# Optimization experiments

Hardware: AMD Instinct MI355X
Metric: run time of the kernel (lower is better)

## Reference

```python
import jax, jax.numpy as jnp
import numpy as np

SEQ = 8192      # sequence_size
EMB = 64        # embedSize
NCLS = 2        # numClasses
NLEAF = 8192    # leaves of a perfect binary tree (13 levels)


def setup_inputs() -> dict:
    key = jax.random.key(0)
    ks = jax.random.split(key, 7)
    s = 0.02  # small init scale so 13 stacked relu-linears stay numerically sane
    return {
        "leaf_seqs": jax.random.normal(ks[0], (NLEAF, SEQ), jnp.float32),
        "emb_W": jax.random.normal(ks[1], (EMB, SEQ), jnp.float32) * s,
        "emb_b": jax.random.normal(ks[2], (EMB,), jnp.float32) * s,
        "W_W": jax.random.normal(ks[3], (EMB, 2 * EMB), jnp.float32) * s,
        "W_b": jax.random.normal(ks[4], (EMB,), jnp.float32) * s,
        "proj_W": jax.random.normal(ks[5], (NCLS, EMB), jnp.float32) * s,
        "proj_b": jax.random.normal(ks[6], (NCLS,), jnp.float32) * s,
    }


def reference(leaf_seqs, emb_W, emb_b, W_W, W_b, proj_W, proj_b):
    # Leaves: relu(embedding(seq)) for every leaf, batched. [NLEAF, EMB]
    h = jax.nn.relu(jnp.einsum('ns,es->ne', leaf_seqs, emb_W) + emb_b)
    # Internal nodes: combine adjacent sibling pairs level by level
    # (left-to-right recursion over a perfect binary tree == adjacent pairing).
    depth = int(np.log2(NLEAF))  # 13 levels, static Python loop
    for _ in range(depth):
        pair = jnp.concatenate([h[0::2], h[1::2]], axis=1)  # [N/2, 2*EMB]
        h = jax.nn.relu(jnp.einsum('nc,ec->ne', pair, W_W) + W_b)
    # Root: projection logits, [1, NCLS] (forward() only emits the root).
    return jnp.einsum('ne,ce->nc', h, proj_W) + proj_b
```

## Files before the change

### kernel.cpp

```cpp
#include <hip/hip_runtime.h>

#define SEQ   8192
#define EMB   64
#define NLEAF 8192
#define KQ    2048
#define KT    64
#define NT    (KQ / KT)

typedef __attribute__((ext_vector_type(4))) float        f32x4;
typedef __attribute__((ext_vector_type(4))) unsigned int u32x4;

__device__ __forceinline__ unsigned rne_pair(float x, float y) {
    const unsigned ux = __float_as_uint(x), uy = __float_as_uint(y);
    const unsigned rx = (ux + 0x7fffu + ((ux >> 16) & 1u)) >> 16;
    const unsigned ry = (uy + 0x7fffu + ((uy >> 16) & 1u)) & 0xffff0000u;
    return rx | ry;
}

__device__ __forceinline__ void mfma16(f32x4& d, const u32x4 a, const u32x4 b) {
    asm("v_mfma_f32_16x16x32_bf16 %0, %1, %2, %0" : "+v"(d) : "v"(a), "v"(b));
}

__device__ __forceinline__ u32x4 frag_rne(const float* buf, int row, int kk) {
    const int c = kk >> 2;
    const int s = row & 7;
    const char* base = (const char*)buf + row * 256;
    const f32x4 v0 = *(const f32x4*)(base + 16 * (c ^ s));
    const f32x4 v1 = *(const f32x4*)(base + 16 * ((c + 1) ^ s));
    u32x4 h;
    h[0] = rne_pair(v0.x, v0.y);
    h[1] = rne_pair(v0.z, v0.w);
    h[2] = rne_pair(v1.x, v1.y);
    h[3] = rne_pair(v1.z, v1.w);
    return h;
}

#define GLDS16(gp, lp) \
    __builtin_amdgcn_global_load_lds( \
        (const __attribute__((address_space(1))) void*)(gp), \
        (__attribute__((address_space(3))) void*)(lp), 16, 0, 0)

__global__ __launch_bounds__(256) void k_cvtW(const float* __restrict__ W,
                                              unsigned* __restrict__ Wt)
{
    const int gid  = blockIdx.x * 256 + threadIdx.x;
    const int chsw = gid & 7;
    const int row  = (gid >> 3) & 63;
    const int t    = (gid >> 9) & 31;
    const int q    = gid >> 14;
    const int c    = chsw ^ (row & 7);
    const float* src = W + (size_t)row * SEQ + q * KQ + t * KT + c * 8;
    const f32x4 a = *(const f32x4*)(src);
    const f32x4 b = *(const f32x4*)(src + 4);
    u32x4 v;
    v[0] = rne_pair(a.x, a.y);
    v[1] = rne_pair(a.z, a.w);
    v[2] = rne_pair(b.x, b.y);
    v[3] = rne_pair(b.z, b.w);
    u32x4* dst = (u32x4*)(Wt + ((q * 32 + t) * 512 + row * 8 + chsw) * 4);
    *dst = v;
}

__global__ __launch_bounds__(256, 2) void k_gemm(
        const float* __restrict__ A, const char* __restrict__ Wt,
        float* __restrict__ P)
{
    __shared__ float sA[3][64 * 64];
    __shared__ char  sW[3][8192];

    const int tid  = threadIdx.x;
    const int lane = tid & 63;
    const int wid  = tid >> 6;

    const int g     = blockIdx.x >> 2;
    const int q     = blockIdx.x & 3;
    const int gl0   = g * 64;
    const int kbase = q * KQ;

    const int lr = lane >> 4;
    const int lc = lane & 15;

    const float* pA0;
    const float* pA1;
    const float* pA2;
    const float* pA3;
    {
        const int r0 = wid * 16 + 0 * 4 + lr;
        const int r1 = wid * 16 + 1 * 4 + lr;
        const int r2 = wid * 16 + 2 * 4 + lr;
        const int r3 = wid * 16 + 3 * 4 + lr;
        pA0 = A + (size_t)(gl0 + r0) * SEQ + kbase + (lc ^ (r0 & 7)) * 4;
        pA1 = A + (size_t)(gl0 + r1) * SEQ + kbase + (lc ^ (r1 & 7)) * 4;
        pA2 = A + (size_t)(gl0 + r2) * SEQ + kbase + (lc ^ (r2 & 7)) * 4;
        pA3 = A + (size_t)(gl0 + r3) * SEQ + kbase + (lc ^ (r3 & 7)) * 4;
    }
    const char* pW = Wt + (size_t)(q * 32) * 8192 + (2 * wid) * 1024 + lane * 16;

    const int fr = lane & 15;
    const int fq = lane >> 4;

    f32x4 acc0 = {0.f, 0.f, 0.f, 0.f};
    f32x4 acc1 = {0.f, 0.f, 0.f, 0.f};
    f32x4 acc2 = {0.f, 0.f, 0.f, 0.f};
    f32x4 acc3 = {0.f, 0.f, 0.f, 0.f};

#define STAGE(bi_) do { \
    char* wdst = (char*)&sW[bi_][0] + 2 * wid * 1024; \
    GLDS16(pW, wdst); \
    GLDS16(pW + 1024, wdst + 1024); \
    pW += 8192; \
    GLDS16(pA0, &sA[bi_][(wid * 16 + 0) * 64]); \
    GLDS16(pA1, &sA[bi_][(wid * 16 + 4) * 64]); \
    GLDS16(pA2, &sA[bi_][(wid * 16 + 8) * 64]); \
    GLDS16(pA3, &sA[bi_][(wid * 16 + 12) * 64]); \
    pA0 += KT; pA1 += KT; pA2 += KT; pA3 += KT; \
} while (0)

#define COMPUTE(bi_) do { \
    const float* bufA_ = &sA[bi_][0]; \
    const char*  bufW_ = &sW[bi_][0]; \
    _Pragma("unroll") \
    for (int k32 = 0; k32 < 2; ++k32) { \
        const u32x4 af = frag_rne(bufA_, wid * 16 + fr, k32 * 32 + fq * 8); \
        const int baddr = fr * 128 + 16 * ((k32 * 4 + fq) ^ (fr & 7)); \
        const u32x4 b0 = *(const u32x4*)(bufW_ + baddr); \
        const u32x4 b1 = *(const u32x4*)(bufW_ + 2048 + baddr); \
        const u32x4 b2 = *(const u32x4*)(bufW_ + 4096 + baddr); \
        const u32x4 b3 = *(const u32x4*)(bufW_ + 6144 + baddr); \
        mfma16(acc0, af, b0); \
        mfma16(acc1, af, b1); \
        mfma16(acc2, af, b2); \
        mfma16(acc3, af, b3); \
    } \
} while (0)

    STAGE(0);
    STAGE(1);

    int bcur = 0, bnxt = 1, bfut = 2;
    #pragma unroll 1
    for (int t = 0; t < NT; ++t) {
        if (t + 1 < NT) asm volatile("s_waitcnt vmcnt(6)" ::: "memory");
        else            asm volatile("s_waitcnt vmcnt(0)" ::: "memory");
        __builtin_amdgcn_s_barrier();
        __builtin_amdgcn_sched_barrier(0);
        if (t + 2 < NT) STAGE(bfut);
        COMPUTE(bcur);
        const int tmp = bcur; bcur = bnxt; bnxt = bfut; bfut = tmp;
    }

#undef STAGE
#undef COMPUTE

    float* Pq = P + (size_t)q * NLEAF * EMB;
    const int row0 = gl0 + wid * 16 + fq * 4;
    #pragma unroll
    for (int r = 0; r < 4; ++r) {
        Pq[(size_t)(row0 + r) * EMB +  0 + fr] = acc0[r];
        Pq[(size_t)(row0 + r) * EMB + 16 + fr] = acc1[r];
        Pq[(size_t)(row0 + r) * EMB + 32 + fr] = acc2[r];
        Pq[(size_t)(row0 + r) * EMB + 48 + fr] = acc3[r];
    }
}

__device__ __forceinline__ void load_Wt(float (*Wt)[132],
                                        const float* __restrict__ WW, int tid) {
    const int e  = tid >> 2;
    const int c0 = (tid & 3) * 32;
    #pragma unroll
    for (int j = 0; j < 32; j += 4)
        *(f32x4*)&Wt[e][c0 + j] = *(const f32x4*)&WW[e * 128 + c0 + j];
}

__device__ __forceinline__ float hsum4(const f32x4 a) {
    return a.x + a.y + a.z + a.w;
}

__device__ __forceinline__ float* tree_levels(float* bufA, float* bufB,
        const float (*Wt)[132], float wb, int n0, int nlv, int tid)
{
    const int lane = tid & 63;
    const int wid  = tid >> 6;
    float* src = bufA;
    float* dst = bufB;
    int n = n0;
    for (int lvl = 0; lvl < nlv; ++lvl) {
        const int nodes = n >> 1;
        for (int base = wid * 4; base < nodes; base += 16) {
            const int cnt = (nodes - base < 4) ? (nodes - base) : 4;
            if (cnt == 4) {
                f32x4 ac0 = {0.f,0.f,0.f,0.f}, ac1 = ac0, ac2 = ac0, ac3 = ac0;
                const float* x0 = src + (2 * (base + 0)) * 68;
                const float* x1 = src + (2 * (base + 1)) * 68;
                const float* x2 = src + (2 * (base + 2)) * 68;
                const float* x3 = src + (2 * (base + 3)) * 68;
                #pragma unroll
                for (int j = 0; j < 32; ++j) {
                    const f32x4 w4 = *(const f32x4*)&Wt[lane][4 * j];
                    const int off = (j < 16) ? (4 * j) : (68 + 4 * (j - 16));
                    ac0 += w4 * *(const f32x4*)(x0 + off);
                    ac1 += w4 * *(const f32x4*)(x1 + off);
                    ac2 += w4 * *(const f32x4*)(x2 + off);
                    ac3 += w4 * *(const f32x4*)(x3 + off);
                }
                dst[(base + 0) * 68 + lane] = fmaxf(wb + hsum4(ac0), 0.f);
                dst[(base + 1) * 68 + lane] = fmaxf(wb + hsum4(ac1), 0.f);
                dst[(base + 2) * 68 + lane] = fmaxf(wb + hsum4(ac2), 0.f);
                dst[(base + 3) * 68 + lane] = fmaxf(wb + hsum4(ac3), 0.f);
            } else {
                for (int u = 0; u < cnt; ++u) {
                    f32x4 ac = {0.f, 0.f, 0.f, 0.f};
                    const float* x = src + (2 * (base + u)) * 68;
                    #pragma unroll
                    for (int j = 0; j < 32; ++j) {
                        const f32x4 w4 = *(const f32x4*)&Wt[lane][4 * j];
                        const int off = (j < 16) ? (4 * j) : (68 + 4 * (j - 16));
                        ac += w4 * *(const f32x4*)(x + off);
                    }
                    dst[(base + u) * 68 + lane] = fmaxf(wb + hsum4(ac), 0.f);
                }
            }
        }
        __syncthreads();
        float* tswp = src; src = dst; dst = tswp;
        n = nodes;
    }
    return src;
}

__global__ __launch_bounds__(256) void k_tree32(const float* __restrict__ P,
        const float* __restrict__ eb, const float* __restrict__ WW,
        const float* __restrict__ Wb, float* __restrict__ roots)
{
    __shared__ float hA[32][68];
    __shared__ float hB[16][68];
    __shared__ float Wt[64][132];
    const int tid = threadIdx.x;
    const int b   = blockIdx.x;
    load_Wt(Wt, WW, tid);
    {
        const int lf = tid >> 3;
        const int e0 = (tid & 7) * 8;
        const size_t base = (size_t)(b * 32 + lf) * EMB + e0;
        f32x4 s0 = *(const f32x4*)&P[base];
        f32x4 s1 = *(const f32x4*)&P[base + 4];
        s0 += *(const f32x4*)&P[(size_t)1 * NLEAF * EMB + base];
        s1 += *(const f32x4*)&P[(size_t)1 * NLEAF * EMB + base + 4];
        s0 += *(const f32x4*)&P[(size_t)2 * NLEAF * EMB + base];
        s1 += *(const f32x4*)&P[(size_t)2 * NLEAF * EMB + base + 4];
        s0 += *(const f32x4*)&P[(size_t)3 * NLEAF * EMB + base];
        s1 += *(const f32x4*)&P[(size_t)3 * NLEAF * EMB + base + 4];
        s0 += *(const f32x4*)&eb[e0];
        s1 += *(const f32x4*)&eb[e0 + 4];
        s0.x = fmaxf(s0.x, 0.f); s0.y = fmaxf(s0.y, 0.f);
        s0.z = fmaxf(s0.z, 0.f); s0.w = fmaxf(s0.w, 0.f);
        s1.x = fmaxf(s1.x, 0.f); s1.y = fmaxf(s1.y, 0.f);
        s1.z = fmaxf(s1.z, 0.f); s1.w = fmaxf(s1.w, 0.f);
        *(f32x4*)&hA[lf][e0]     = s0;
        *(f32x4*)&hA[lf][e0 + 4] = s1;
    }
    const float wb = Wb[tid & 63];
    __syncthreads();
    float* root = tree_levels(&hA[0][0], &hB[0][0], Wt, wb, 32, 5, tid);
    if (tid < 64) roots[b * 64 + tid] = root[tid];
}

__global__ __launch_bounds__(256) void k_tree16(const float* __restrict__ in,
        const float* __restrict__ WW, const float* __restrict__ Wb,
        float* __restrict__ outv)
{
    __shared__ float hA[32][68];
    __shared__ float hB[16][68];
    __shared__ float Wt[64][132];
    const int tid = threadIdx.x;
    load_Wt(Wt, WW, tid);
    {
        const int r  = tid >> 4;
        const int e0 = (tid & 15) * 4;
        *(f32x4*)&hA[r][e0] =
            *(const f32x4*)&in[(size_t)(blockIdx.x * 16 + r) * EMB + e0];
    }
    const float wb = Wb[tid & 63];
    __syncthreads();
    float* root = tree_levels(&hA[0][0], &hB[0][0], Wt, wb, 16, 4, tid);
    if (tid < 64) outv[blockIdx.x * 64 + tid] = root[tid];
}

__global__ __launch_bounds__(256) void k_root(const float* __restrict__ in,
        const float* __restrict__ WW, const float* __restrict__ Wb,
        const float* __restrict__ pW, const float* __restrict__ pb,
        float* __restrict__ out)
{
    __shared__ float hA[32][68];
    __shared__ float hB[16][68];
    __shared__ float Wt[64][132];
    const int tid = threadIdx.x;
    load_Wt(Wt, WW, tid);
    {
        const int r  = tid >> 4;
        const int e0 = (tid & 15) * 4;
        *(f32x4*)&hA[r][e0] = *(const f32x4*)&in[(size_t)r * EMB + e0];
    }
    const float wb = Wb[tid & 63];
    __syncthreads();
    float* root = tree_levels(&hA[0][0], &hB[0][0], Wt, wb, 16, 4, tid);
    if (tid < 64) {
        const float hv = root[tid];
        float t0 = hv * pW[tid];
        float t1 = hv * pW[64 + tid];
        #pragma unroll
        for (int off = 32; off > 0; off >>= 1) {
            t0 += __shfl_down(t0, off);
            t1 += __shfl_down(t1, off);
        }
        if (tid == 0) { out[0] = t0 + pb[0]; out[1] = t1 + pb[1]; }
    }
}

extern "C" void kernel_launch(void* const* d_in, const int* in_sizes, int n_in,
                              void* d_out, int out_size, void* d_ws, size_t ws_size,
                              hipStream_t stream)
{
    const float* A  = (const float*)d_in[0];
    const float* eW = (const float*)d_in[1];
    const float* eb = (const float*)d_in[2];
    const float* WW = (const float*)d_in[3];
    const float* Wb = (const float*)d_in[4];
    const float* pW = (const float*)d_in[5];
    const float* pb = (const float*)d_in[6];
    float* out = (float*)d_out;

    float* P     = (float*)d_ws;
    float* roots = P + (size_t)4 * NLEAF * EMB;
    float* l9    = roots + 256 * EMB;
    char*  Wtil  = (char*)d_ws + (size_t)16 * 1024 * 1024;

    k_cvtW  <<<dim3(256), dim3(256), 0, stream>>>(eW, (unsigned*)Wtil);
    k_gemm  <<<dim3(512), dim3(256), 0, stream>>>(A, Wtil, P);
    k_tree32<<<dim3(256), dim3(256), 0, stream>>>(P, eb, WW, Wb, roots);
    k_tree16<<<dim3(16),  dim3(256), 0, stream>>>(roots, WW, Wb, l9);
    k_root  <<<dim3(1),   dim3(256), 0, stream>>>(l9, WW, Wb, pW, pb, out);
}
```

Before: 82.58 us.

## Fuse last two tree kernels via atomic last-block-done and transpose W smem layout

```diff
diff --git a/kernel.cpp b/kernel.cpp
--- a/kernel.cpp
+++ b/kernel.cpp
@@ -163,13 +163,15 @@
     }
 }
 
-__device__ __forceinline__ void load_Wt(float (*Wt)[132],
-                                        const float* __restrict__ WW, int tid) {
-    const int e  = tid >> 2;
-    const int c0 = (tid & 3) * 32;
+__device__ __forceinline__ void load_WtV(f32x4 (*WtV)[64],
+                                         const float* __restrict__ WW, int tid) {
+    const int e  = tid & 63;
+    const int jg = tid >> 6;
     #pragma unroll
-    for (int j = 0; j < 32; j += 4)
-        *(f32x4*)&Wt[e][c0 + j] = *(const f32x4*)&WW[e * 128 + c0 + j];
+    for (int u = 0; u < 8; ++u) {
+        const int j = jg * 8 + u;
+        WtV[j][e] = *(const f32x4*)&WW[e * 128 + 4 * j];
+    }
 }
 
 __device__ __forceinline__ float hsum4(const f32x4 a) {
@@ -177,7 +179,7 @@
 }
 
 __device__ __forceinline__ float* tree_levels(float* bufA, float* bufB,
-        const float (*Wt)[132], float wb, int n0, int nlv, int tid)
+        const f32x4 (*WtV)[64], float wb, int n0, int nlv, int tid)
 {
     const int lane = tid & 63;
     const int wid  = tid >> 6;
@@ -196,7 +198,7 @@
                 const float* x3 = src + (2 * (base + 3)) * 68;
                 #pragma unroll
                 for (int j = 0; j < 32; ++j) {
-                    const f32x4 w4 = *(const f32x4*)&Wt[lane][4 * j];
+                    const f32x4 w4 = WtV[j][lane];
                     const int off = (j < 16) ? (4 * j) : (68 + 4 * (j - 16));
                     ac0 += w4 * *(const f32x4*)(x0 + off);
                     ac1 += w4 * *(const f32x4*)(x1 + off);
@@ -213,7 +215,7 @@
                     const float* x = src + (2 * (base + u)) * 68;
                     #pragma unroll
                     for (int j = 0; j < 32; ++j) {
-                        const f32x4 w4 = *(const f32x4*)&Wt[lane][4 * j];
+                        const f32x4 w4 = WtV[j][lane];
                         const int off = (j < 16) ? (4 * j) : (68 + 4 * (j - 16));
                         ac += w4 * *(const f32x4*)(x + off);
                     }
@@ -234,10 +236,10 @@
 {
     __shared__ float hA[32][68];
     __shared__ float hB[16][68];
-    __shared__ float Wt[64][132];
+    __shared__ f32x4 WtV[32][64];
     const int tid = threadIdx.x;
     const int b   = blockIdx.x;
-    load_Wt(Wt, WW, tid);
+    load_WtV(WtV, WW, tid);
     {
         const int lf = tid >> 3;
         const int e0 = (tid & 7) * 8;
@@ -261,19 +263,22 @@
     }
     const float wb = Wb[tid & 63];
     __syncthreads();
-    float* root = tree_levels(&hA[0][0], &hB[0][0], Wt, wb, 32, 5, tid);
+    float* root = tree_levels(&hA[0][0], &hB[0][0], WtV, wb, 32, 5, tid);
     if (tid < 64) roots[b * 64 + tid] = root[tid];
 }
 
-__global__ __launch_bounds__(256) void k_tree16(const float* __restrict__ in,
+__global__ __launch_bounds__(256) void k_tail(const float* __restrict__ in,
         const float* __restrict__ WW, const float* __restrict__ Wb,
-        float* __restrict__ outv)
+        const float* __restrict__ pW, const float* __restrict__ pb,
+        float* __restrict__ l9, unsigned* __restrict__ cnt,
+        float* __restrict__ out)
 {
     __shared__ float hA[32][68];
     __shared__ float hB[16][68];
-    __shared__ float Wt[64][132];
+    __shared__ f32x4 WtV[32][64];
+    __shared__ int sflag;
     const int tid = threadIdx.x;
-    load_Wt(Wt, WW, tid);
+    load_WtV(WtV, WW, tid);
     {
         const int r  = tid >> 4;
         const int e0 = (tid & 15) * 4;
@@ -282,28 +287,30 @@
     }
     const float wb = Wb[tid & 63];
     __syncthreads();
-    float* root = tree_levels(&hA[0][0], &hB[0][0], Wt, wb, 16, 4, tid);
-    if (tid < 64) outv[blockIdx.x * 64 + tid] = root[tid];
-}
-
-__global__ __launch_bounds__(256) void k_root(const float* __restrict__ in,
-        const float* __restrict__ WW, const float* __restrict__ Wb,
-        const float* __restrict__ pW, const float* __restrict__ pb,
-        float* __restrict__ out)
-{
-    __shared__ float hA[32][68];
-    __shared__ float hB[16][68];
-    __shared__ float Wt[64][132];
-    const int tid = threadIdx.x;
-    load_Wt(Wt, WW, tid);
+    float* root = tree_levels(&hA[0][0], &hB[0][0], WtV, wb, 16, 4, tid);
+    if (tid < 64)
+        __hip_atomic_store(&l9[blockIdx.x * 64 + tid], root[tid],
+                           __ATOMIC_RELAXED, __HIP_MEMORY_SCOPE_AGENT);
+    __threadfence();
+    if (tid == 0)
+        sflag = (__hip_atomic_fetch_add(cnt, 1u, __ATOMIC_ACQ_REL,
+                                        __HIP_MEMORY_SCOPE_AGENT) == 15u);
+    __syncthreads();
+    if (!sflag) return;
+
+    __builtin_amdgcn_fence(__ATOMIC_ACQUIRE, "agent");
     {
         const int r  = tid >> 4;
         const int e0 = (tid & 15) * 4;
-        *(f32x4*)&hA[r][e0] = *(const f32x4*)&in[(size_t)r * EMB + e0];
-    }
-    const float wb = Wb[tid & 63];
+        f32x4 v;
+        v.x = __hip_atomic_load(&l9[r * 64 + e0 + 0], __ATOMIC_RELAXED, __HIP_MEMORY_SCOPE_AGENT);
+        v.y = __hip_atomic_load(&l9[r * 64 + e0 + 1], __ATOMIC_RELAXED, __HIP_MEMORY_SCOPE_AGENT);
+        v.z = __hip_atomic_load(&l9[r * 64 + e0 + 2], __ATOMIC_RELAXED, __HIP_MEMORY_SCOPE_AGENT);
+        v.w = __hip_atomic_load(&l9[r * 64 + e0 + 3], __ATOMIC_RELAXED, __HIP_MEMORY_SCOPE_AGENT);
+        *(f32x4*)&hA[r][e0] = v;
+    }
     __syncthreads();
-    float* root = tree_levels(&hA[0][0], &hB[0][0], Wt, wb, 16, 4, tid);
+    root = tree_levels(&hA[0][0], &hB[0][0], WtV, wb, 16, 4, tid);
     if (tid < 64) {
         const float hv = root[tid];
         float t0 = hv * pW[tid];
@@ -330,14 +337,16 @@
     const float* pb = (const float*)d_in[6];
     float* out = (float*)d_out;
 
-    float* P     = (float*)d_ws;
-    float* roots = P + (size_t)4 * NLEAF * EMB;
-    float* l9    = roots + 256 * EMB;
-    char*  Wtil  = (char*)d_ws + (size_t)16 * 1024 * 1024;
-
+    float*    P     = (float*)d_ws;
+    float*    roots = P + (size_t)4 * NLEAF * EMB;
+    float*    l9    = roots + 256 * EMB;
+    unsigned* cnt   = (unsigned*)((char*)d_ws + 8 * 1024 * 1024 + 72 * 1024);
+    char*     Wtil  = (char*)d_ws + (size_t)16 * 1024 * 1024;
+
+    hipMemsetAsync(cnt, 0, 64, stream);
     k_cvtW  <<<dim3(256), dim3(256), 0, stream>>>(eW, (unsigned*)Wtil);
     k_gemm  <<<dim3(512), dim3(256), 0, stream>>>(A, Wtil, P);
     k_tree32<<<dim3(256), dim3(256), 0, stream>>>(P, eb, WW, Wb, roots);
-    k_tree16<<<dim3(16),  dim3(256), 0, stream>>>(roots, WW, Wb, l9);
-    k_root  <<<dim3(1),   dim3(256), 0, stream>>>(l9, WW, Wb, pW, pb, out);
-}
+    k_tail  <<<dim3(16),  dim3(256), 0, stream>>>(roots, WW, Wb, pW, pb,
+                                                  l9, cnt, out);
+}
```

New measurement: 85.73 us. 1.04x slower.

## Load A fragments directly from global into registers, bypassing LDS staging

Applied to the files above, without the earlier changes.

```diff
diff --git a/kernel.cpp b/kernel.cpp
--- a/kernel.cpp
+++ b/kernel.cpp
@@ -19,20 +19,6 @@
 
 __device__ __forceinline__ void mfma16(f32x4& d, const u32x4 a, const u32x4 b) {
     asm("v_mfma_f32_16x16x32_bf16 %0, %1, %2, %0" : "+v"(d) : "v"(a), "v"(b));
-}
-
-__device__ __forceinline__ u32x4 frag_rne(const float* buf, int row, int kk) {
-    const int c = kk >> 2;
-    const int s = row & 7;
-    const char* base = (const char*)buf + row * 256;
-    const f32x4 v0 = *(const f32x4*)(base + 16 * (c ^ s));
-    const f32x4 v1 = *(const f32x4*)(base + 16 * ((c + 1) ^ s));
-    u32x4 h;
-    h[0] = rne_pair(v0.x, v0.y);
-    h[1] = rne_pair(v0.z, v0.w);
-    h[2] = rne_pair(v1.x, v1.y);
-    h[3] = rne_pair(v1.z, v1.w);
-    return h;
 }
 
 #define GLDS16(gp, lp) \
@@ -65,8 +51,7 @@
         const float* __restrict__ A, const char* __restrict__ Wt,
         float* __restrict__ P)
 {
-    __shared__ float sA[3][64 * 64];
-    __shared__ char  sW[3][8192];
+    __shared__ char sW[3][8192];
 
     const int tid  = threadIdx.x;
     const int lane = tid & 63;
@@ -77,80 +62,86 @@
     const int gl0   = g * 64;
     const int kbase = q * KQ;
 
-    const int lr = lane >> 4;
-    const int lc = lane & 15;
-
-    const float* pA0;
-    const float* pA1;
-    const float* pA2;
-    const float* pA3;
-    {
-        const int r0 = wid * 16 + 0 * 4 + lr;
-        const int r1 = wid * 16 + 1 * 4 + lr;
-        const int r2 = wid * 16 + 2 * 4 + lr;
-        const int r3 = wid * 16 + 3 * 4 + lr;
-        pA0 = A + (size_t)(gl0 + r0) * SEQ + kbase + (lc ^ (r0 & 7)) * 4;
-        pA1 = A + (size_t)(gl0 + r1) * SEQ + kbase + (lc ^ (r1 & 7)) * 4;
-        pA2 = A + (size_t)(gl0 + r2) * SEQ + kbase + (lc ^ (r2 & 7)) * 4;
-        pA3 = A + (size_t)(gl0 + r3) * SEQ + kbase + (lc ^ (r3 & 7)) * 4;
-    }
-    const char* pW = Wt + (size_t)(q * 32) * 8192 + (2 * wid) * 1024 + lane * 16;
-
     const int fr = lane & 15;
     const int fq = lane >> 4;
+
+    const float* pA = A + (size_t)(gl0 + wid * 16 + fr) * SEQ + kbase + fq * 8;
+    const char* pW = Wt + (size_t)(q * 32) * 8192 + (2 * wid) * 1024 + lane * 16;
 
     f32x4 acc0 = {0.f, 0.f, 0.f, 0.f};
     f32x4 acc1 = {0.f, 0.f, 0.f, 0.f};
     f32x4 acc2 = {0.f, 0.f, 0.f, 0.f};
     f32x4 acc3 = {0.f, 0.f, 0.f, 0.f};
 
-#define STAGE(bi_) do { \
+    f32x4 a0c0, a0c1, a0c2, a0c3;
+    f32x4 a1c0, a1c1, a1c2, a1c3;
+
+#define STAGEW(bi_) do { \
     char* wdst = (char*)&sW[bi_][0] + 2 * wid * 1024; \
     GLDS16(pW, wdst); \
     GLDS16(pW + 1024, wdst + 1024); \
     pW += 8192; \
-    GLDS16(pA0, &sA[bi_][(wid * 16 + 0) * 64]); \
-    GLDS16(pA1, &sA[bi_][(wid * 16 + 4) * 64]); \
-    GLDS16(pA2, &sA[bi_][(wid * 16 + 8) * 64]); \
-    GLDS16(pA3, &sA[bi_][(wid * 16 + 12) * 64]); \
-    pA0 += KT; pA1 += KT; pA2 += KT; pA3 += KT; \
 } while (0)
 
-#define COMPUTE(bi_) do { \
-    const float* bufA_ = &sA[bi_][0]; \
-    const char*  bufW_ = &sW[bi_][0]; \
-    _Pragma("unroll") \
-    for (int k32 = 0; k32 < 2; ++k32) { \
-        const u32x4 af = frag_rne(bufA_, wid * 16 + fr, k32 * 32 + fq * 8); \
-        const int baddr = fr * 128 + 16 * ((k32 * 4 + fq) ^ (fr & 7)); \
-        const u32x4 b0 = *(const u32x4*)(bufW_ + baddr); \
-        const u32x4 b1 = *(const u32x4*)(bufW_ + 2048 + baddr); \
-        const u32x4 b2 = *(const u32x4*)(bufW_ + 4096 + baddr); \
-        const u32x4 b3 = *(const u32x4*)(bufW_ + 6144 + baddr); \
-        mfma16(acc0, af, b0); \
-        mfma16(acc1, af, b1); \
-        mfma16(acc2, af, b2); \
-        mfma16(acc3, af, b3); \
-    } \
+#define LOADA(c0_, c1_, c2_, c3_) do { \
+    c0_ = *(const f32x4*)(pA); \
+    c1_ = *(const f32x4*)(pA + 4); \
+    c2_ = *(const f32x4*)(pA + 32); \
+    c3_ = *(const f32x4*)(pA + 36); \
+    pA += KT; \
 } while (0)
 
-    STAGE(0);
-    STAGE(1);
+#define COMPUTE(c0_, c1_, c2_, c3_, bi_) do { \
+    const char* bufW_ = &sW[bi_][0]; \
+    u32x4 af; \
+    af[0] = rne_pair(c0_.x, c0_.y); \
+    af[1] = rne_pair(c0_.z, c0_.w); \
+    af[2] = rne_pair(c1_.x, c1_.y); \
+    af[3] = rne_pair(c1_.z, c1_.w); \
+    { const int baddr = fr * 128 + 16 * (fq ^ (fr & 7)); \
+      mfma16(acc0, af, *(const u32x4*)(bufW_ + baddr)); \
+      mfma16(acc1, af, *(const u32x4*)(bufW_ + 2048 + baddr)); \
+      mfma16(acc2, af, *(const u32x4*)(bufW_ + 4096 + baddr)); \
+      mfma16(acc3, af, *(const u32x4*)(bufW_ + 6144 + baddr)); } \
+    af[0] = rne_pair(c2_.x, c2_.y); \
+    af[1] = rne_pair(c2_.z, c2_.w); \
+    af[2] = rne_pair(c3_.x, c3_.y); \
+    af[3] = rne_pair(c3_.z, c3_.w); \
+    { const int baddr = fr * 128 + 16 * ((4 + fq) ^ (fr & 7)); \
+      mfma16(acc0, af, *(const u32x4*)(bufW_ + baddr)); \
+      mfma16(acc1, af, *(const u32x4*)(bufW_ + 2048 + baddr)); \
+      mfma16(acc2, af, *(const u32x4*)(bufW_ + 4096 + baddr)); \
+      mfma16(acc3, af, *(const u32x4*)(bufW_ + 6144 + baddr)); } \
+} while (0)
+
+#define PHASE(t_, c0_, c1_, c2_, c3_) do { \
+    if ((t_) < NT - 1) asm volatile("s_waitcnt vmcnt(6)" ::: "memory"); \
+    else               asm volatile("s_waitcnt vmcnt(0)" ::: "memory"); \
+    __builtin_amdgcn_s_barrier(); \
+    __builtin_amdgcn_sched_barrier(0); \
+    const bool more2_ = ((t_) + 2 < NT); \
+    if (more2_) STAGEW(bfut); \
+    COMPUTE(c0_, c1_, c2_, c3_, bcur); \
+    if (more2_) LOADA(c0_, c1_, c2_, c3_); \
+    const int tmp_ = bcur; bcur = bnxt; bnxt = bfut; bfut = tmp_; \
+} while (0)
+
+    STAGEW(0);
+    LOADA(a0c0, a0c1, a0c2, a0c3);
+    STAGEW(1);
+    LOADA(a1c0, a1c1, a1c2, a1c3);
 
     int bcur = 0, bnxt = 1, bfut = 2;
     #pragma unroll 1
-    for (int t = 0; t < NT; ++t) {
-        if (t + 1 < NT) asm volatile("s_waitcnt vmcnt(6)" ::: "memory");
-        else            asm volatile("s_waitcnt vmcnt(0)" ::: "memory");
-        __builtin_amdgcn_s_barrier();
-        __builtin_amdgcn_sched_barrier(0);
-        if (t + 2 < NT) STAGE(bfut);
-        COMPUTE(bcur);
-        const int tmp = bcur; bcur = bnxt; bnxt = bfut; bfut = tmp;
-    }
-
-#undef STAGE
+    for (int i = 0; i < NT / 2; ++i) {
+        PHASE(2 * i,     a0c0, a0c1, a0c2, a0c3);
+        PHASE(2 * i + 1, a1c0, a1c1, a1c2, a1c3);
+    }
+
+#undef STAGEW
+#undef LOADA
 #undef COMPUTE
+#undef PHASE
 
     float* Pq = P + (size_t)q * NLEAF * EMB;
     const int row0 = gl0 + wid * 16 + fq * 4;
```

Result: slower. 84.46 us (+2.3%).
